# Performance work log

Measured on AMD Instinct MI355X. Metric: run time of the kernel, lower is better.

## Reference

```python
import jax, jax.numpy as jnp
import numpy as np

N, P, T, H, W = 16, 16, 8, 224, 224


def setup_inputs() -> dict:
    key = jax.random.key(0)
    k1, k2 = jax.random.split(key)
    # binary {0,1} group masks (torch version takes LongTensor; only nonzero pattern matters)
    groups_pred = jax.random.randint(k1, (N, P, H, W), 0, 2).astype(jnp.float32)
    groups_true = jax.random.randint(k2, (N, T, H, W), 0, 2).astype(jnp.float32)
    return {"groups_pred": groups_pred, "groups_true": groups_true}


def reference(groups_pred, groups_true):
    # binarize, matching torch's .bool().long()
    Gp = (groups_pred != 0).astype(jnp.float32)  # (N,P,H,W)
    Gt = (groups_true != 0).astype(jnp.float32)  # (N,T,H,W)

    # pairwise intersection via batched GEMM over flattened HW
    inters = jnp.einsum('nphw,nthw->npt', Gp, Gt)          # (N,P,T)
    sp = Gp.sum(axis=(-1, -2))                              # (N,P)
    st = Gt.sum(axis=(-1, -2))                              # (N,T)
    # |A u B| = |A| + |B| - |A n B| for binary masks == clamp(A+B,0,1).sum()
    unions = sp[:, :, None] + st[:, None, :] - inters       # (N,P,T)

    ious = inters / unions
    ious = jnp.where(jnp.isfinite(ious), ious, 0.0)
    iou_maxs = ious.max(axis=-1)                            # (N,P)

    # weight each predicted mask by its best IoU, sum over P
    pred_aligns_sum = jnp.einsum('nphw,np->nhw', Gp, iou_maxs)  # (N,H,W)
    score = pred_aligns_sum / Gp.sum(axis=1)                    # (N,H,W)
    score = jnp.where(jnp.isfinite(score), score, 0.0)
    return score.mean(axis=(1, 2))                              # (N,)
```

## Files before the change

kernel.cpp:

```cpp
#include <hip/hip_runtime.h>

#define NN 16
#define PB 16
#define TB 8
#define HWPX 50176
#define WORDS 784
#define GROUPS 196

__global__ void zero_kernel(float* __restrict__ inters, float* __restrict__ sp,
                            float* __restrict__ st, float* __restrict__ out) {
    int i = threadIdx.x + blockIdx.x * blockDim.x;
    if (i < NN * PB * TB) inters[i] = 0.f;
    if (i < NN * PB) sp[i] = 0.f;
    if (i < NN * TB) st[i] = 0.f;
    if (i < NN) out[i] = 0.f;
}

__global__ void pack_kernel(const float* __restrict__ pred,
                            const float* __restrict__ truth,
                            unsigned long long* __restrict__ PP,
                            unsigned long long* __restrict__ PT) {
    const int totalGroups = (NN * PB + NN * TB) * GROUPS;
    const int wavesPerBlock = blockDim.x >> 6;
    const int waveId = blockIdx.x * wavesPerBlock + (threadIdx.x >> 6);
    const int lane = threadIdx.x & 63;
    const int nWaves = gridDim.x * wavesPerBlock;

    for (int G = waveId; G < totalGroups; G += nWaves) {
        int plane = G / GROUPS;
        int g = G - plane * GROUPS;
        const float* src;
        unsigned long long* dst;
        if (plane < NN * PB) {
            src = pred + (size_t)plane * HWPX;
            dst = PP + (size_t)plane * WORDS;
        } else {
            int q = plane - NN * PB;
            src = truth + (size_t)q * HWPX;
            dst = PT + (size_t)q * WORDS;
        }
        const float4 v = *(const float4*)(src + g * 256 + lane * 4);
        unsigned long long b0 = __ballot(v.x != 0.0f);
        unsigned long long b1 = __ballot(v.y != 0.0f);
        unsigned long long b2 = __ballot(v.z != 0.0f);
        unsigned long long b3 = __ballot(v.w != 0.0f);
        if (lane == 0) {
            dst[g * 4 + 0] = b0;
            dst[g * 4 + 1] = b1;
            dst[g * 4 + 2] = b2;
            dst[g * 4 + 3] = b3;
        }
    }
}

#define K2_SPLIT 28
__global__ void inters_kernel(const unsigned long long* __restrict__ PP,
                              const unsigned long long* __restrict__ PT,
                              float* __restrict__ inters,
                              float* __restrict__ sp, float* __restrict__ st) {
    const int n = blockIdx.x / K2_SPLIT;
    const int s = blockIdx.x % K2_SPLIT;
    const int p = threadIdx.x >> 3;
    const int t = threadIdx.x & 7;
    const unsigned long long* pp = PP + ((size_t)n * PB + p) * WORDS;
    const unsigned long long* pt = PT + ((size_t)n * TB + t) * WORDS;
    const int w0 = s * (WORDS / K2_SPLIT);
    int acc = 0, accp = 0, acct = 0;
#pragma unroll 4
    for (int w = w0; w < w0 + (WORDS / K2_SPLIT); ++w) {
        unsigned long long a = pp[w];
        unsigned long long b = pt[w];
        acc += __popcll(a & b);
        accp += __popcll(a);
        acct += __popcll(b);
    }
    atomicAdd(&inters[((size_t)n * PB + p) * TB + t], (float)acc);
    if (t == 0) atomicAdd(&sp[n * PB + p], (float)accp);
    if (p == 0) atomicAdd(&st[n * TB + t], (float)acct);
}

#define K3_CH 16
__global__ void score_kernel(const unsigned long long* __restrict__ PP,
                             const float* __restrict__ inters,
                             const float* __restrict__ sp,
                             const float* __restrict__ st,
                             float* __restrict__ out) {
    const int n = blockIdx.x / K3_CH;
    const int c = blockIdx.x % K3_CH;
    __shared__ float ioumax_s[PB];
    __shared__ float redbuf[4];

    if (threadIdx.x < PB) {
        int p = threadIdx.x;
        float spv = sp[n * PB + p];
        float m = 0.f;
#pragma unroll
        for (int t = 0; t < TB; ++t) {
            float iv = inters[((size_t)n * PB + p) * TB + t];
            float un = spv + st[n * TB + t] - iv;
            float iou = un > 0.f ? iv / un : 0.f;
            m = fmaxf(m, iou);
        }
        ioumax_s[p] = m;
    }
    __syncthreads();

    const int lane = threadIdx.x & 63;
    const int wv = threadIdx.x >> 6;
    const int wpb = WORDS / K3_CH;
    float sum = 0.f;
    for (int w = c * wpb + wv; w < (c + 1) * wpb; w += 4) {
        float num = 0.f, den = 0.f;
#pragma unroll
        for (int p = 0; p < PB; ++p) {
            unsigned long long m = PP[((size_t)n * PB + p) * WORDS + w];
            float b = (float)((m >> lane) & 1ull);
            den += b;
            num += b * ioumax_s[p];
        }
        sum += den > 0.f ? num / den : 0.f;
    }
#pragma unroll
    for (int off = 32; off > 0; off >>= 1) sum += __shfl_down(sum, off, 64);
    if (lane == 0) redbuf[wv] = sum;
    __syncthreads();
    if (threadIdx.x == 0) {
        float tot = redbuf[0] + redbuf[1] + redbuf[2] + redbuf[3];
        atomicAdd(&out[n], tot * (1.0f / (float)HWPX));
    }
}

extern "C" void kernel_launch(void* const* d_in, const int* in_sizes, int n_in,
                              void* d_out, int out_size, void* d_ws, size_t ws_size,
                              hipStream_t stream) {
    const float* pred = (const float*)d_in[0];
    const float* truth = (const float*)d_in[1];
    float* out = (float*)d_out;

    unsigned long long* PP = (unsigned long long*)d_ws;
    unsigned long long* PT = PP + (size_t)NN * PB * WORDS;
    float* inters = (float*)(PT + (size_t)NN * TB * WORDS);
    float* sp = inters + NN * PB * TB;
    float* st = sp + NN * PB;

    zero_kernel<<<2, 1024, 0, stream>>>(inters, sp, st, out);
    pack_kernel<<<1024, 256, 0, stream>>>(pred, truth, PP, PT);
    inters_kernel<<<NN * K2_SPLIT, 128, 0, stream>>>(PP, PT, inters, sp, st);
    score_kernel<<<NN * K3_CH, 256, 0, stream>>>(PP, inters, sp, st, out);
}
```

Measured before the change: 122.4 us.

## Fuse intersection and score kernels, fold zeroing into pack kernel

Drops the zero kernel by clearing the output inside the pack kernel, and merges the intersection and score kernels into one. In the merged kernel each block recomputes the full per-image intersection counts in shared memory rather than combining partial counts through global atomics. The pack kernel's grid doubles, and its lane-0 stores become two 16-byte stores. The division in the score loop is replaced by a small reciprocal table lookup. This cuts two launches and the global atomics, at the cost of every chunk block redundantly recomputing the intersections (16x redundant popcount work per image).

```diff
diff --git a/kernel.cpp b/kernel.cpp
--- a/kernel.cpp
+++ b/kernel.cpp
@@ -5,28 +5,24 @@
 #define TB 8
 #define HWPX 50176
 #define WORDS 784
+#define HALF 392
 #define GROUPS 196
+#define TOTAL_GROUPS ((NN * PB + NN * TB) * GROUPS)
+#define K2_CH 16
+#define WPC (WORDS / K2_CH)
 
-__global__ void zero_kernel(float* __restrict__ inters, float* __restrict__ sp,
-                            float* __restrict__ st, float* __restrict__ out) {
-    int i = threadIdx.x + blockIdx.x * blockDim.x;
-    if (i < NN * PB * TB) inters[i] = 0.f;
-    if (i < NN * PB) sp[i] = 0.f;
-    if (i < NN * TB) st[i] = 0.f;
-    if (i < NN) out[i] = 0.f;
-}
+__global__ __launch_bounds__(256) void pack_kernel(
+        const float* __restrict__ pred, const float* __restrict__ truth,
+        unsigned long long* __restrict__ PP, unsigned long long* __restrict__ PT,
+        float* __restrict__ out) {
+    if (blockIdx.x == 0 && threadIdx.x < NN) out[threadIdx.x] = 0.f;
 
-__global__ void pack_kernel(const float* __restrict__ pred,
-                            const float* __restrict__ truth,
-                            unsigned long long* __restrict__ PP,
-                            unsigned long long* __restrict__ PT) {
-    const int totalGroups = (NN * PB + NN * TB) * GROUPS;
     const int wavesPerBlock = blockDim.x >> 6;
     const int waveId = blockIdx.x * wavesPerBlock + (threadIdx.x >> 6);
     const int lane = threadIdx.x & 63;
     const int nWaves = gridDim.x * wavesPerBlock;
 
-    for (int G = waveId; G < totalGroups; G += nWaves) {
+    for (int G = waveId; G < TOTAL_GROUPS; G += nWaves) {
         int plane = G / GROUPS;
         int g = G - plane * GROUPS;
         const float* src;
@@ -45,106 +41,111 @@
         unsigned long long b2 = __ballot(v.z != 0.0f);
         unsigned long long b3 = __ballot(v.w != 0.0f);
         if (lane == 0) {
-            dst[g * 4 + 0] = b0;
-            dst[g * 4 + 1] = b1;
-            dst[g * 4 + 2] = b2;
-            dst[g * 4 + 3] = b3;
+            ulonglong2 lo, hi;
+            lo.x = b0; lo.y = b1; hi.x = b2; hi.y = b3;
+            ((ulonglong2*)dst)[g * 2 + 0] = lo;
+            ((ulonglong2*)dst)[g * 2 + 1] = hi;
         }
     }
 }
 
-#define K2_SPLIT 28
-__global__ void inters_kernel(const unsigned long long* __restrict__ PP,
-                              const unsigned long long* __restrict__ PT,
-                              float* __restrict__ inters,
-                              float* __restrict__ sp, float* __restrict__ st) {
-    const int n = blockIdx.x / K2_SPLIT;
-    const int s = blockIdx.x % K2_SPLIT;
-    const int p = threadIdx.x >> 3;
-    const int t = threadIdx.x & 7;
-    const unsigned long long* pp = PP + ((size_t)n * PB + p) * WORDS;
-    const unsigned long long* pt = PT + ((size_t)n * TB + t) * WORDS;
-    const int w0 = s * (WORDS / K2_SPLIT);
+__global__ __launch_bounds__(256) void fused_kernel(
+        const unsigned long long* __restrict__ PP,
+        const unsigned long long* __restrict__ PT,
+        float* __restrict__ out) {
+    const int n = blockIdx.x / K2_CH;
+    const int c = blockIdx.x % K2_CH;
+    const int tid = threadIdx.x;
+
+    __shared__ int inters_s[PB * TB];
+    __shared__ int sp_s[PB];
+    __shared__ int st_s[TB];
+    __shared__ float ioumax_s[PB];
+    __shared__ float rcp_s[17];
+    __shared__ float red_s[4];
+
+    if (tid < 17) rcp_s[tid] = tid ? 1.0f / (float)tid : 0.0f;
+
+    const int pair = tid >> 1;
+    const int h = tid & 1;
+    const int p = pair >> 3, t = pair & 7;
+    const ulonglong2* pp2 =
+        (const ulonglong2*)(PP + ((size_t)n * PB + p) * WORDS + h * HALF);
+    const ulonglong2* pt2 =
+        (const ulonglong2*)(PT + ((size_t)n * TB + t) * WORDS + h * HALF);
     int acc = 0, accp = 0, acct = 0;
 #pragma unroll 4
-    for (int w = w0; w < w0 + (WORDS / K2_SPLIT); ++w) {
-        unsigned long long a = pp[w];
-        unsigned long long b = pt[w];
-        acc += __popcll(a & b);
-        accp += __popcll(a);
-        acct += __popcll(b);
+    for (int i = 0; i < HALF / 2; ++i) {
+        ulonglong2 a = pp2[i];
+        ulonglong2 b = pt2[i];
+        acc  += __popcll(a.x & b.x) + __popcll(a.y & b.y);
+        accp += __popcll(a.x) + __popcll(a.y);
+        acct += __popcll(b.x) + __popcll(b.y);
     }
-    atomicAdd(&inters[((size_t)n * PB + p) * TB + t], (float)acc);
-    if (t == 0) atomicAdd(&sp[n * PB + p], (float)accp);
-    if (p == 0) atomicAdd(&st[n * TB + t], (float)acct);
-}
-
-#define K3_CH 16
-__global__ void score_kernel(const unsigned long long* __restrict__ PP,
-                             const float* __restrict__ inters,
-                             const float* __restrict__ sp,
-                             const float* __restrict__ st,
-                             float* __restrict__ out) {
-    const int n = blockIdx.x / K3_CH;
-    const int c = blockIdx.x % K3_CH;
-    __shared__ float ioumax_s[PB];
-    __shared__ float redbuf[4];
-
-    if (threadIdx.x < PB) {
-        int p = threadIdx.x;
-        float spv = sp[n * PB + p];
-        float m = 0.f;
-#pragma unroll
-        for (int t = 0; t < TB; ++t) {
-            float iv = inters[((size_t)n * PB + p) * TB + t];
-            float un = spv + st[n * TB + t] - iv;
-            float iou = un > 0.f ? iv / un : 0.f;
-            m = fmaxf(m, iou);
-        }
-        ioumax_s[p] = m;
+    acc  += __shfl_xor(acc, 1, 64);
+    accp += __shfl_xor(accp, 1, 64);
+    acct += __shfl_xor(acct, 1, 64);
+    if (h == 0) {
+        inters_s[pair] = acc;
+        if (t == 0) sp_s[p] = accp;
+        if (p == 0) st_s[t] = acct;
     }
     __syncthreads();
 
-    const int lane = threadIdx.x & 63;
-    const int wv = threadIdx.x >> 6;
-    const int wpb = WORDS / K3_CH;
+    if (tid < PB) {
+        float spv = (float)sp_s[tid];
+        float m = 0.f;
+#pragma unroll
+        for (int tt = 0; tt < TB; ++tt) {
+            float iv = (float)inters_s[tid * TB + tt];
+            float un = spv + (float)st_s[tt] - iv;
+            m = fmaxf(m, un > 0.f ? iv / un : 0.f);
+        }
+        ioumax_s[tid] = m;
+    }
+    __syncthreads();
+
+    float iom[PB];
+#pragma unroll
+    for (int q = 0; q < PB; ++q) iom[q] = ioumax_s[q];
+
+    const int lane = tid & 63;
+    const int wv = tid >> 6;
+    const unsigned long long* base = PP + (size_t)n * PB * WORDS;
     float sum = 0.f;
-    for (int w = c * wpb + wv; w < (c + 1) * wpb; w += 4) {
-        float num = 0.f, den = 0.f;
+    for (int w = c * WPC + wv; w < (c + 1) * WPC; w += 4) {
+        float num = 0.f;
+        unsigned int den = 0;
 #pragma unroll
-        for (int p = 0; p < PB; ++p) {
-            unsigned long long m = PP[((size_t)n * PB + p) * WORDS + w];
-            float b = (float)((m >> lane) & 1ull);
-            den += b;
-            num += b * ioumax_s[p];
+        for (int q = 0; q < PB; ++q) {
+            unsigned long long m = base[(size_t)q * WORDS + w];
+            unsigned int bit = (unsigned int)(m >> lane) & 1u;
+            den += bit;
+            num = fmaf((float)bit, iom[q], num);
         }
-        sum += den > 0.f ? num / den : 0.f;
+        sum += num * rcp_s[den];
     }
+
 #pragma unroll
     for (int off = 32; off > 0; off >>= 1) sum += __shfl_down(sum, off, 64);
-    if (lane == 0) redbuf[wv] = sum;
+    if (lane == 0) red_s[wv] = sum;
     __syncthreads();
-    if (threadIdx.x == 0) {
-        float tot = redbuf[0] + redbuf[1] + redbuf[2] + redbuf[3];
-        atomicAdd(&out[n], tot * (1.0f / (float)HWPX));
+    if (tid == 0) {
+        atomicAdd(&out[n],
+                  (red_s[0] + red_s[1] + red_s[2] + red_s[3]) * (1.0f / (float)HWPX));
     }
 }
 
 extern "C" void kernel_launch(void* const* d_in, const int* in_sizes, int n_in,
                               void* d_out, int out_size, void* d_ws, size_t ws_size,
                               hipStream_t stream) {
-    const float* pred = (const float*)d_in[0];
+    const float* pred  = (const float*)d_in[0];
     const float* truth = (const float*)d_in[1];
     float* out = (float*)d_out;
 
     unsigned long long* PP = (unsigned long long*)d_ws;
     unsigned long long* PT = PP + (size_t)NN * PB * WORDS;
-    float* inters = (float*)(PT + (size_t)NN * TB * WORDS);
-    float* sp = inters + NN * PB * TB;
-    float* st = sp + NN * PB;
 
-    zero_kernel<<<2, 1024, 0, stream>>>(inters, sp, st, out);
-    pack_kernel<<<1024, 256, 0, stream>>>(pred, truth, PP, PT);
-    inters_kernel<<<NN * K2_SPLIT, 128, 0, stream>>>(PP, PT, inters, sp, st);
-    score_kernel<<<NN * K3_CH, 256, 0, stream>>>(PP, inters, sp, st, out);
+    pack_kernel<<<2048, 256, 0, stream>>>(pred, truth, PP, PT, out);
+    fused_kernel<<<NN * K2_CH, 256, 0, stream>>>(PP, PT, out);
 }
```

New measurement: 132.1 us. +8.0%, slower.
